# Kernel optimization log

Measured on AMD Instinct MI355X. Metric: run time of the kernel, lower is better.

Reference implementation:

```python
import jax, jax.numpy as jnp
import numpy as np

B, S, E, H = 2, 2048, 2048, 16
D = E // H

def setup_inputs() -> dict:
    key = jax.random.key(0)
    ks = jax.random.split(key, 9)
    sc = 1.0 / np.sqrt(E)
    return {
        "x":  jax.random.normal(ks[0], (B, S, E), jnp.float32),
        "Wq": jax.random.normal(ks[1], (E, E), jnp.float32) * sc,
        "bq": jax.random.normal(ks[2], (E,), jnp.float32) * 0.01,
        "Wk": jax.random.normal(ks[3], (E, E), jnp.float32) * sc,
        "bk": jax.random.normal(ks[4], (E,), jnp.float32) * 0.01,
        "Wv": jax.random.normal(ks[5], (E, E), jnp.float32) * sc,
        "bv": jax.random.normal(ks[6], (E,), jnp.float32) * 0.01,
        "Wo": jax.random.normal(ks[7], (E, E), jnp.float32) * sc,
        "bo": jax.random.normal(ks[8], (E,), jnp.float32) * 0.01,
    }

def _split_heads(t):
    # [B,S,E] -> [B,H,S,D]
    return t.reshape(B, S, H, D).transpose(0, 2, 1, 3)

def reference(x, Wq, bq, Wk, bk, Wv, bv, Wo, bo):
    # projections (nn.Linear: y = x @ W^T + b)
    q = _split_heads(x @ Wq.T + bq)
    k = _split_heads(x @ Wk.T + bk)
    v = _split_heads(x @ Wv.T + bv)

    # scaled causal attention; scale uses k.size(-1) == head_dim D
    scores = jnp.einsum("bhqd,bhkd->bhqk", q, k) / jnp.sqrt(jnp.asarray(D, q.dtype))
    causal = jnp.tril(jnp.ones((S, S), bool))  # [S,S]
    scores = jnp.where(causal[None, None, :, :], scores, -jnp.inf)
    # training path subtracts row max before softmax (no-op under stable softmax)
    scores = scores - jnp.max(scores, axis=-1, keepdims=True)
    attn = jax.nn.softmax(scores, axis=-1)
    # dropout_rate = 0.0 -> identity
    ctx = jnp.einsum("bhqk,bhkd->bhqd", attn, v)

    # merge heads [B,H,S,D] -> [B,S,E], final projection
    out = ctx.transpose(0, 2, 1, 3).reshape(B, S, E)
    return out @ Wo.T + bo
```

## Files before the change

kernel.cpp:

```cpp
#include <hip/hip_runtime.h>

typedef unsigned short u16;
typedef __attribute__((ext_vector_type(4))) float f32x4;
typedef __attribute__((ext_vector_type(8))) short s16x8;
typedef __attribute__((ext_vector_type(4))) unsigned short u16x4;

#define MFMA16(a, b, c) __builtin_amdgcn_mfma_f32_16x16x32_bf16((a), (b), (c), 0, 0, 0)

__device__ __forceinline__ u16 f2bf(float f) {
  union { float f; unsigned u; } v; v.f = f;
  unsigned u = v.u;
  u += 0x7fffu + ((u >> 16) & 1u);
  return (u16)(u >> 16);
}

__device__ __forceinline__ void gl_lds16(const void* g, void* l) {
  __builtin_amdgcn_global_load_lds(
      (const __attribute__((address_space(1))) void*)g,
      (__attribute__((address_space(3))) void*)l, 16, 0, 0);
}

__global__ void cast6(const float* __restrict__ x,
                      const float* __restrict__ w0, const float* __restrict__ w1,
                      const float* __restrict__ w2, const float* __restrict__ w3,
                      u16* __restrict__ ws) {
  const int y = blockIdx.y;
  const float* src;
  u16* dst;
  if (y < 2) { src = x + (size_t)y * 4194304; dst = ws + (size_t)y * 4194304; }
  else {
    src = (y == 2) ? w0 : (y == 3) ? w1 : (y == 4) ? w2 : w3;
    dst = ws + 8388608 + (size_t)(y - 2) * 4194304;
  }
  const int i = blockIdx.x * 256 + threadIdx.x;
  f32x4 v = ((const f32x4*)src)[i];
  u16x4 o;
#pragma unroll
  for (int e = 0; e < 4; ++e) o[e] = f2bf(v[e]);
  ((u16x4*)dst)[i] = o;
}

__global__ __launch_bounds__(256, 2) void gemm_qkv(
    const u16* __restrict__ A,
    const u16* __restrict__ W0, const u16* __restrict__ W1, const u16* __restrict__ W2,
    const float* __restrict__ b0, const float* __restrict__ b1, const float* __restrict__ b2,
    u16* __restrict__ Qo, u16* __restrict__ Ko, u16* __restrict__ Vo) {
  constexpr int Kd = 2048;
  __shared__ __align__(16) u16 smem[17408];
  u16* sA = smem;
  u16* sB = smem + 8192;
  const int z = blockIdx.z;
  const u16* Bw = (z == 0) ? W0 : (z == 1) ? W1 : W2;
  const float* bias = (z == 0) ? b0 : (z == 1) ? b1 : b2;

  const int tid = threadIdx.x;
  const int lane = tid & 63, w = tid >> 6;
  const int ln = lane & 15, quad = lane >> 4;
  const int m0 = blockIdx.y * 128, n0 = blockIdx.x * 128;
  const int wm = (w >> 1) * 64, wn = (w & 1) * 64;

  f32x4 acc[4][4] = {};
  const int srow = lane >> 3;
  const int scol = (lane & 7) * 8;

  for (int k0 = 0; k0 < Kd; k0 += 64) {
#pragma unroll
    for (int c = 0; c < 4; ++c) {
      const int chunk = c * 4 + w;
      const int row = chunk * 8 + srow;
      gl_lds16(A + (size_t)(m0 + row) * Kd + k0 + scol, (char*)sA + chunk * 1024);
      gl_lds16(Bw + (size_t)(n0 + row) * Kd + k0 + scol, (char*)sB + chunk * 1024);
    }
    __syncthreads();
#pragma unroll
    for (int kk = 0; kk < 64; kk += 32) {
      s16x8 af[4], bf[4];
#pragma unroll
      for (int t = 0; t < 4; ++t) {
        af[t] = *(const s16x8*)&sA[(wm + t * 16 + ln) * 64 + kk + quad * 8];
        bf[t] = *(const s16x8*)&sB[(wn + t * 16 + ln) * 64 + kk + quad * 8];
      }
#pragma unroll
      for (int tm = 0; tm < 4; ++tm)
#pragma unroll
        for (int tn = 0; tn < 4; ++tn)
          acc[tm][tn] = MFMA16(af[tm], bf[tn], acc[tm][tn]);
    }
    __syncthreads();
  }

  if (z < 2) {
    u16* out = (z == 0) ? Qo : Ko;
    const float scale = (z == 0) ? 0.08838834764831845f : 1.0f;
#pragma unroll
    for (int tn = 0; tn < 4; ++tn) {
      const int n = n0 + wn + tn * 16 + ln;
      const float bv = bias[n];
      const int h = n >> 7, d = n & 127;
#pragma unroll
      for (int tm = 0; tm < 4; ++tm)
#pragma unroll
        for (int r = 0; r < 4; ++r) {
          const int m = m0 + wm + tm * 16 + quad * 4 + r;
          const int b = m >> 11, s = m & 2047;
          out[(((size_t)(b * 16 + h)) << 18) + ((size_t)s << 7) + d] =
              f2bf((acc[tm][tn][r] + bv) * scale);
        }
    }
  } else {
    u16* Tt = smem;
#pragma unroll
    for (int tn = 0; tn < 4; ++tn) {
      const int n = n0 + wn + tn * 16 + ln;
      const float bv = bias[n];
      const int dl = wn + tn * 16 + ln;
#pragma unroll
      for (int tm = 0; tm < 4; ++tm)
#pragma unroll
        for (int r = 0; r < 4; ++r) {
          const int sl = wm + tm * 16 + quad * 4 + r;
          Tt[dl * 136 + sl] = f2bf(acc[tm][tn][r] + bv);
        }
    }
    __syncthreads();
    const int h = n0 >> 7, b = m0 >> 11, s0 = m0 & 2047;
#pragma unroll
    for (int c = 0; c < 8; ++c) {
      const int id = c * 256 + tid;
      const int row = id >> 4, cc = id & 15;
      s16x8 vr = *(const s16x8*)&Tt[row * 136 + cc * 8];
      *(s16x8*)&Vo[(((size_t)((b * 16 + h) * 128 + row)) << 11) + s0 + cc * 8] = vr;
    }
  }
}

__global__ __launch_bounds__(256, 2) void gemm_out(const u16* __restrict__ A,
                                                   const u16* __restrict__ Bw,
                                                   const float* __restrict__ bias,
                                                   float* __restrict__ out) {
  constexpr int Kd = 2048;
  __shared__ __align__(16) u16 sA[128 * 64];
  __shared__ __align__(16) u16 sB[128 * 64];
  const int tid = threadIdx.x;
  const int lane = tid & 63, w = tid >> 6;
  const int ln = lane & 15, quad = lane >> 4;
  const int m0 = blockIdx.y * 128, n0 = blockIdx.x * 128;
  const int wm = (w >> 1) * 64, wn = (w & 1) * 64;

  f32x4 acc[4][4] = {};
  const int srow = lane >> 3;
  const int scol = (lane & 7) * 8;

  for (int k0 = 0; k0 < Kd; k0 += 64) {
#pragma unroll
    for (int c = 0; c < 4; ++c) {
      const int chunk = c * 4 + w;
      const int row = chunk * 8 + srow;
      gl_lds16(A + (size_t)(m0 + row) * Kd + k0 + scol, (char*)sA + chunk * 1024);
      gl_lds16(Bw + (size_t)(n0 + row) * Kd + k0 + scol, (char*)sB + chunk * 1024);
    }
    __syncthreads();
#pragma unroll
    for (int kk = 0; kk < 64; kk += 32) {
      s16x8 af[4], bf[4];
#pragma unroll
      for (int t = 0; t < 4; ++t) {
        af[t] = *(const s16x8*)&sA[(wm + t * 16 + ln) * 64 + kk + quad * 8];
        bf[t] = *(const s16x8*)&sB[(wn + t * 16 + ln) * 64 + kk + quad * 8];
      }
#pragma unroll
      for (int tm = 0; tm < 4; ++tm)
#pragma unroll
        for (int tn = 0; tn < 4; ++tn)
          acc[tm][tn] = MFMA16(af[tm], bf[tn], acc[tm][tn]);
    }
    __syncthreads();
  }
#pragma unroll
  for (int tn = 0; tn < 4; ++tn) {
    const int n = n0 + wn + tn * 16 + ln;
    const float bv = bias[n];
#pragma unroll
    for (int tm = 0; tm < 4; ++tm)
#pragma unroll
      for (int r = 0; r < 4; ++r) {
        const int m = m0 + wm + tm * 16 + quad * 4 + r;
        out[(size_t)m * 2048 + n] = acc[tm][tn][r] + bv;
      }
  }
}

__global__ __launch_bounds__(256, 2) void attn_kernel(const u16* __restrict__ Q,
                                                      const u16* __restrict__ Kp,
                                                      const u16* __restrict__ Vt,
                                                      u16* __restrict__ ctx) {
  __shared__ __align__(16) u16 smem[24576];
  u16* sP = smem;
  u16* sK = smem + 8192;
  u16* sV = smem + 16384;

  const int flat = blockIdx.x + (blockIdx.y << 4);
  const int bh = flat >> 4;
  const int i = (flat < 256) ? (15 - (flat & 15)) : (flat & 15);
  const size_t base = (size_t)bh << 18;

  const int tid = threadIdx.x, lane = tid & 63, w = tid >> 6;
  const int ln = lane & 15, quad = lane >> 4, ln7 = lane & 7;

#pragma unroll
  for (int c = 0; c < 8; ++c) {
    const int chunk0 = (c * 4 + w) * 64;
    const int chunk = chunk0 + lane;
    const int row = chunk >> 4, cc = chunk & 15;
    gl_lds16(Q + base + (size_t)((i * 128 + row) * 128 + ((cc ^ (row & 15)) << 3)),
             (char*)sK + chunk0 * 16);
  }
  __syncthreads();
  s16x8 qf[2][4];
#pragma unroll
  for (int tm = 0; tm < 2; ++tm)
#pragma unroll
    for (int kc = 0; kc < 4; ++kc)
      qf[tm][kc] =
          *(const s16x8*)&sK[(w * 32 + tm * 16 + ln) * 128 + (((kc * 4 + quad) ^ ln) << 3)];
  __syncthreads();

  auto stageK = [&](int j) {
#pragma unroll
    for (int c = 0; c < 4; ++c) {
      const int chunk0 = (c * 4 + w) * 64;
      const int chunk = chunk0 + lane;
      const int row = chunk >> 4, cc = chunk & 15;
      gl_lds16(Kp + base + (size_t)((j * 64 + row) * 128 + ((cc ^ (row & 15)) << 3)),
               (char*)sK + chunk0 * 16);
    }
  };
  auto stageV = [&](int j) {
#pragma unroll
    for (int c = 0; c < 4; ++c) {
      const int chunk0 = (c * 4 + w) * 64;
      const int chunk = chunk0 + lane;
      const int row = chunk >> 3, cc = chunk & 7;
      gl_lds16(Vt + base + (size_t)(row * 2048 + j * 64 + ((cc ^ (row & 7)) << 3)),
               (char*)sV + chunk0 * 16);
    }
  };

  stageK(0);
  stageV(0);
  __syncthreads();

  f32x4 o_acc[2][8] = {};
  float lsum[2][4] = {};
  const int jmax = 2 * i + 1;

  for (int j = 0; j <= jmax; ++j) {
    f32x4 sacc[2][4] = {};
#pragma unroll
    for (int kc = 0; kc < 4; ++kc) {
      s16x8 kf[4];
#pragma unroll
      for (int tn = 0; tn < 4; ++tn)
        kf[tn] = *(const s16x8*)&sK[(tn * 16 + ln) * 128 + (((kc * 4 + quad) ^ ln) << 3)];
#pragma unroll
      for (int tm = 0; tm < 2; ++tm)
#pragma unroll
        for (int tn = 0; tn < 4; ++tn)
          sacc[tm][tn] = MFMA16(qf[tm][kc], kf[tn], sacc[tm][tn]);
    }

    const bool diag = (j >= 2 * i);
#pragma unroll
    for (int tm = 0; tm < 2; ++tm)
#pragma unroll
      for (int tn = 0; tn < 4; ++tn) {
        const int kg = j * 64 + tn * 16 + ln;
#pragma unroll
        for (int r = 0; r < 4; ++r) {
          const int rloc = w * 32 + tm * 16 + quad * 4 + r;
          float pv = __expf(sacc[tm][tn][r]);
          if (diag && kg > i * 128 + rloc) pv = 0.f;
          lsum[tm][r] += pv;
          const int chunk = tn * 2 + (ln >> 3);
          sP[rloc * 64 + ((chunk ^ (rloc & 7)) << 3) + ln7] = f2bf(pv);
        }
      }
    __syncthreads();
    if (j < jmax) stageK(j + 1);

#pragma unroll
    for (int kc = 0; kc < 2; ++kc) {
      s16x8 pf[2], vf[8];
#pragma unroll
      for (int tm = 0; tm < 2; ++tm)
        pf[tm] =
            *(const s16x8*)&sP[(w * 32 + tm * 16 + ln) * 64 + (((kc * 4 + quad) ^ ln7) << 3)];
#pragma unroll
      for (int tn = 0; tn < 8; ++tn)
        vf[tn] = *(const s16x8*)&sV[(tn * 16 + ln) * 64 + (((kc * 4 + quad) ^ ln7) << 3)];
#pragma unroll
      for (int tm = 0; tm < 2; ++tm)
#pragma unroll
        for (int tn = 0; tn < 8; ++tn)
          o_acc[tm][tn] = MFMA16(pf[tm], vf[tn], o_acc[tm][tn]);
    }
    __syncthreads();
    if (j < jmax) stageV(j + 1);
  }

  const int b = bh >> 4, h = bh & 15;
#pragma unroll
  for (int tm = 0; tm < 2; ++tm) {
    float rinv[4];
#pragma unroll
    for (int r = 0; r < 4; ++r) {
      float s = lsum[tm][r];
      s += __shfl_xor(s, 1);
      s += __shfl_xor(s, 2);
      s += __shfl_xor(s, 4);
      s += __shfl_xor(s, 8);
      rinv[r] = __builtin_amdgcn_rcpf(s);
    }
#pragma unroll
    for (int tn = 0; tn < 8; ++tn) {
      const int d = tn * 16 + ln;
#pragma unroll
      for (int r = 0; r < 4; ++r) {
        const int sg = i * 128 + w * 32 + tm * 16 + quad * 4 + r;
        ctx[((size_t)b << 22) + (size_t)sg * 2048 + h * 128 + d] =
            f2bf(o_acc[tm][tn][r] * rinv[r]);
      }
    }
  }
}

extern "C" void kernel_launch(void* const* d_in, const int* in_sizes, int n_in,
                              void* d_out, int out_size, void* d_ws, size_t ws_size,
                              hipStream_t stream) {
  const float* x = (const float*)d_in[0];
  const float* Wq = (const float*)d_in[1];
  const float* bq = (const float*)d_in[2];
  const float* Wk = (const float*)d_in[3];
  const float* bk = (const float*)d_in[4];
  const float* Wv = (const float*)d_in[5];
  const float* bv = (const float*)d_in[6];
  const float* Wo = (const float*)d_in[7];
  const float* bo = (const float*)d_in[8];

  u16* ws = (u16*)d_ws;
  u16* xb = ws;
  u16* Wqb = xb + 8388608;
  u16* Wkb = Wqb + 4194304;
  u16* Wvb = Wkb + 4194304;
  u16* Wob = Wvb + 4194304;
  u16* Qb = Wob + 4194304;
  u16* Kb = Qb + 8388608;
  u16* Vtb = Kb + 8388608;
  u16* ctxb = Vtb + 8388608;

  cast6<<<dim3(4096, 6), 256, 0, stream>>>(x, Wq, Wk, Wv, Wo, ws);

  gemm_qkv<<<dim3(16, 32, 3), 256, 0, stream>>>(xb, Wqb, Wkb, Wvb, bq, bk, bv, Qb, Kb, Vtb);

  attn_kernel<<<dim3(16, 32), 256, 0, stream>>>(Qb, Kb, Vtb, ctxb);

  gemm_out<<<dim3(16, 32), 256, 0, stream>>>(ctxb, Wob, bo, (float*)d_out);
}
```

Before: 391.8 us.

## Swap MFMA operand order for vectorized epilogues and XOR-swizzle GEMM LDS tiles

Measured after the change: 366.8 us. 6.4% less time.

```diff
diff --git a/kernel.cpp b/kernel.cpp
--- a/kernel.cpp
+++ b/kernel.cpp
@@ -40,13 +40,53 @@
   ((u16x4*)dst)[i] = o;
 }
 
+template <int SWAP>
+__device__ __forceinline__ void gemm_core(const u16* __restrict__ A,
+                                          const u16* __restrict__ Bw,
+                                          u16* sA, u16* sB,
+                                          f32x4 (&acc)[4][4],
+                                          int m0, int n0, int tid) {
+  const int lane = tid & 63, w = tid >> 6;
+  const int ln = lane & 15, quad = lane >> 4, ln7 = ln & 7;
+  const int wm = (w >> 1) * 64, wn = (w & 1) * 64;
+  const int srow = lane >> 3;
+  const int scol = (((lane & 7) ^ srow)) * 8;
+
+  for (int k0 = 0; k0 < 2048; k0 += 64) {
+#pragma unroll
+    for (int c = 0; c < 4; ++c) {
+      const int chunk = c * 4 + w;
+      const int row = chunk * 8 + srow;
+      gl_lds16(A + (size_t)(m0 + row) * 2048 + k0 + scol, (char*)sA + chunk * 1024);
+      gl_lds16(Bw + (size_t)(n0 + row) * 2048 + k0 + scol, (char*)sB + chunk * 1024);
+    }
+    __syncthreads();
+#pragma unroll
+    for (int kk = 0; kk < 64; kk += 32) {
+      s16x8 af[4], bf[4];
+      const int g = (kk >> 3) + quad;
+#pragma unroll
+      for (int t = 0; t < 4; ++t) {
+        af[t] = *(const s16x8*)&sA[(wm + t * 16 + ln) * 64 + ((g ^ ln7) << 3)];
+        bf[t] = *(const s16x8*)&sB[(wn + t * 16 + ln) * 64 + ((g ^ ln7) << 3)];
+      }
+#pragma unroll
+      for (int tm = 0; tm < 4; ++tm)
+#pragma unroll
+        for (int tn = 0; tn < 4; ++tn)
+          acc[tm][tn] = SWAP ? MFMA16(bf[tn], af[tm], acc[tm][tn])
+                             : MFMA16(af[tm], bf[tn], acc[tm][tn]);
+    }
+    __syncthreads();
+  }
+}
+
 __global__ __launch_bounds__(256, 2) void gemm_qkv(
     const u16* __restrict__ A,
     const u16* __restrict__ W0, const u16* __restrict__ W1, const u16* __restrict__ W2,
     const float* __restrict__ b0, const float* __restrict__ b1, const float* __restrict__ b2,
     u16* __restrict__ Qo, u16* __restrict__ Ko, u16* __restrict__ Vo) {
-  constexpr int Kd = 2048;
-  __shared__ __align__(16) u16 smem[17408];
+  __shared__ __align__(16) u16 smem[16384];
   u16* sA = smem;
   u16* sB = smem + 8192;
   const int z = blockIdx.z;
@@ -60,76 +100,41 @@
   const int wm = (w >> 1) * 64, wn = (w & 1) * 64;
 
   f32x4 acc[4][4] = {};
-  const int srow = lane >> 3;
-  const int scol = (lane & 7) * 8;
-
-  for (int k0 = 0; k0 < Kd; k0 += 64) {
-#pragma unroll
-    for (int c = 0; c < 4; ++c) {
-      const int chunk = c * 4 + w;
-      const int row = chunk * 8 + srow;
-      gl_lds16(A + (size_t)(m0 + row) * Kd + k0 + scol, (char*)sA + chunk * 1024);
-      gl_lds16(Bw + (size_t)(n0 + row) * Kd + k0 + scol, (char*)sB + chunk * 1024);
-    }
-    __syncthreads();
-#pragma unroll
-    for (int kk = 0; kk < 64; kk += 32) {
-      s16x8 af[4], bf[4];
-#pragma unroll
-      for (int t = 0; t < 4; ++t) {
-        af[t] = *(const s16x8*)&sA[(wm + t * 16 + ln) * 64 + kk + quad * 8];
-        bf[t] = *(const s16x8*)&sB[(wn + t * 16 + ln) * 64 + kk + quad * 8];
-      }
-#pragma unroll
-      for (int tm = 0; tm < 4; ++tm)
-#pragma unroll
-        for (int tn = 0; tn < 4; ++tn)
-          acc[tm][tn] = MFMA16(af[tm], bf[tn], acc[tm][tn]);
-    }
-    __syncthreads();
-  }
-
   if (z < 2) {
+    gemm_core<1>(A, Bw, sA, sB, acc, m0, n0, tid);
     u16* out = (z == 0) ? Qo : Ko;
     const float scale = (z == 0) ? 0.08838834764831845f : 1.0f;
+#pragma unroll
+    for (int tn = 0; tn < 4; ++tn) {
+      const int n_base = n0 + wn + tn * 16 + quad * 4;
+      const f32x4 bv = *(const f32x4*)&bias[n_base];
+      const int h = n_base >> 7, dl = n_base & 127;
+#pragma unroll
+      for (int tm = 0; tm < 4; ++tm) {
+        const int m = m0 + wm + tm * 16 + ln;
+        const int b = m >> 11, s = m & 2047;
+        u16x4 ov;
+#pragma unroll
+        for (int r = 0; r < 4; ++r) ov[r] = f2bf((acc[tm][tn][r] + bv[r]) * scale);
+        *(u16x4*)&out[(((size_t)(b * 16 + h)) << 18) + ((size_t)s << 7) + dl] = ov;
+      }
+    }
+  } else {
+    gemm_core<0>(A, Bw, sA, sB, acc, m0, n0, tid);
+    const int b = m0 >> 11;
 #pragma unroll
     for (int tn = 0; tn < 4; ++tn) {
       const int n = n0 + wn + tn * 16 + ln;
       const float bv = bias[n];
-      const int h = n >> 7, d = n & 127;
-#pragma unroll
-      for (int tm = 0; tm < 4; ++tm)
-#pragma unroll
-        for (int r = 0; r < 4; ++r) {
-          const int m = m0 + wm + tm * 16 + quad * 4 + r;
-          const int b = m >> 11, s = m & 2047;
-          out[(((size_t)(b * 16 + h)) << 18) + ((size_t)s << 7) + d] =
-              f2bf((acc[tm][tn][r] + bv) * scale);
-        }
-    }
-  } else {
-    u16* Tt = smem;
-#pragma unroll
-    for (int tn = 0; tn < 4; ++tn) {
-      const int n = n0 + wn + tn * 16 + ln;
-      const float bv = bias[n];
-      const int dl = wn + tn * 16 + ln;
-#pragma unroll
-      for (int tm = 0; tm < 4; ++tm)
-#pragma unroll
-        for (int r = 0; r < 4; ++r) {
-          const int sl = wm + tm * 16 + quad * 4 + r;
-          Tt[dl * 136 + sl] = f2bf(acc[tm][tn][r] + bv);
-        }
-    }
-    __syncthreads();
-    const int h = n0 >> 7, b = m0 >> 11, s0 = m0 & 2047;
-#pragma unroll
-    for (int c = 0; c < 8; ++c) {
-      const int id = c * 256 + tid;
-      const int row = id >> 4, cc = id & 15;
-      s16x8 vr = *(const s16x8*)&Tt[row * 136 + cc * 8];
-      *(s16x8*)&Vo[(((size_t)((b * 16 + h) * 128 + row)) << 11) + s0 + cc * 8] = vr;
+      const int h = n >> 7, dl = n & 127;
+#pragma unroll
+      for (int tm = 0; tm < 4; ++tm) {
+        const int s_base = (m0 & 2047) + wm + tm * 16 + quad * 4;
+        u16x4 ov;
+#pragma unroll
+        for (int r = 0; r < 4; ++r) ov[r] = f2bf(acc[tm][tn][r] + bv);
+        *(u16x4*)&Vo[(((size_t)((b * 16 + h) * 128 + dl)) << 11) + s_base] = ov;
+      }
     }
   }
 }
@@ -138,9 +143,9 @@
                                                    const u16* __restrict__ Bw,
                                                    const float* __restrict__ bias,
                                                    float* __restrict__ out) {
-  constexpr int Kd = 2048;
-  __shared__ __align__(16) u16 sA[128 * 64];
-  __shared__ __align__(16) u16 sB[128 * 64];
+  __shared__ __align__(16) u16 smem[16384];
+  u16* sA = smem;
+  u16* sB = smem + 8192;
   const int tid = threadIdx.x;
   const int lane = tid & 63, w = tid >> 6;
   const int ln = lane & 15, quad = lane >> 4;
@@ -148,45 +153,19 @@
   const int wm = (w >> 1) * 64, wn = (w & 1) * 64;
 
   f32x4 acc[4][4] = {};
-  const int srow = lane >> 3;
-  const int scol = (lane & 7) * 8;
-
-  for (int k0 = 0; k0 < Kd; k0 += 64) {
-#pragma unroll
-    for (int c = 0; c < 4; ++c) {
-      const int chunk = c * 4 + w;
-      const int row = chunk * 8 + srow;
-      gl_lds16(A + (size_t)(m0 + row) * Kd + k0 + scol, (char*)sA + chunk * 1024);
-      gl_lds16(Bw + (size_t)(n0 + row) * Kd + k0 + scol, (char*)sB + chunk * 1024);
-    }
-    __syncthreads();
-#pragma unroll
-    for (int kk = 0; kk < 64; kk += 32) {
-      s16x8 af[4], bf[4];
-#pragma unroll
-      for (int t = 0; t < 4; ++t) {
-        af[t] = *(const s16x8*)&sA[(wm + t * 16 + ln) * 64 + kk + quad * 8];
-        bf[t] = *(const s16x8*)&sB[(wn + t * 16 + ln) * 64 + kk + quad * 8];
-      }
-#pragma unroll
-      for (int tm = 0; tm < 4; ++tm)
-#pragma unroll
-        for (int tn = 0; tn < 4; ++tn)
-          acc[tm][tn] = MFMA16(af[tm], bf[tn], acc[tm][tn]);
-    }
-    __syncthreads();
-  }
+  gemm_core<1>(A, Bw, sA, sB, acc, m0, n0, tid);
 #pragma unroll
   for (int tn = 0; tn < 4; ++tn) {
-    const int n = n0 + wn + tn * 16 + ln;
-    const float bv = bias[n];
-#pragma unroll
-    for (int tm = 0; tm < 4; ++tm)
-#pragma unroll
-      for (int r = 0; r < 4; ++r) {
-        const int m = m0 + wm + tm * 16 + quad * 4 + r;
-        out[(size_t)m * 2048 + n] = acc[tm][tn][r] + bv;
-      }
+    const int n_base = n0 + wn + tn * 16 + quad * 4;
+    const f32x4 bv = *(const f32x4*)&bias[n_base];
+#pragma unroll
+    for (int tm = 0; tm < 4; ++tm) {
+      const int m = m0 + wm + tm * 16 + ln;
+      f32x4 ov;
+#pragma unroll
+      for (int r = 0; r < 4; ++r) ov[r] = acc[tm][tn][r] + bv[r];
+      *(f32x4*)&out[(size_t)m * 2048 + n_base] = ov;
+    }
   }
 }
 
@@ -218,11 +197,11 @@
   __syncthreads();
   s16x8 qf[2][4];
 #pragma unroll
-  for (int tm = 0; tm < 2; ++tm)
+  for (int qt = 0; qt < 2; ++qt)
 #pragma unroll
     for (int kc = 0; kc < 4; ++kc)
-      qf[tm][kc] =
-          *(const s16x8*)&sK[(w * 32 + tm * 16 + ln) * 128 + (((kc * 4 + quad) ^ ln) << 3)];
+      qf[qt][kc] =
+          *(const s16x8*)&sK[(w * 32 + qt * 16 + ln) * 128 + (((kc * 4 + quad) ^ ln) << 3)];
   __syncthreads();
 
   auto stageK = [&](int j) {
@@ -250,88 +229,89 @@
   stageV(0);
   __syncthreads();
 
-  f32x4 o_acc[2][8] = {};
-  float lsum[2][4] = {};
+  f32x4 o_acc[8][2] = {};
+  float lsum[2] = {0.f, 0.f};
   const int jmax = 2 * i + 1;
+  const int qg = i * 128 + w * 32 + ln;
 
   for (int j = 0; j <= jmax; ++j) {
-    f32x4 sacc[2][4] = {};
+    f32x4 sacc[4][2] = {};
 #pragma unroll
     for (int kc = 0; kc < 4; ++kc) {
       s16x8 kf[4];
 #pragma unroll
-      for (int tn = 0; tn < 4; ++tn)
-        kf[tn] = *(const s16x8*)&sK[(tn * 16 + ln) * 128 + (((kc * 4 + quad) ^ ln) << 3)];
-#pragma unroll
-      for (int tm = 0; tm < 2; ++tm)
-#pragma unroll
-        for (int tn = 0; tn < 4; ++tn)
-          sacc[tm][tn] = MFMA16(qf[tm][kc], kf[tn], sacc[tm][tn]);
+      for (int kt = 0; kt < 4; ++kt)
+        kf[kt] = *(const s16x8*)&sK[(kt * 16 + ln) * 128 + (((kc * 4 + quad) ^ ln) << 3)];
+#pragma unroll
+      for (int kt = 0; kt < 4; ++kt)
+#pragma unroll
+        for (int qt = 0; qt < 2; ++qt)
+          sacc[kt][qt] = MFMA16(kf[kt], qf[qt][kc], sacc[kt][qt]);
     }
 
     const bool diag = (j >= 2 * i);
 #pragma unroll
-    for (int tm = 0; tm < 2; ++tm)
-#pragma unroll
-      for (int tn = 0; tn < 4; ++tn) {
-        const int kg = j * 64 + tn * 16 + ln;
+    for (int kt = 0; kt < 4; ++kt)
+#pragma unroll
+      for (int qt = 0; qt < 2; ++qt) {
+        u16x4 pk;
 #pragma unroll
         for (int r = 0; r < 4; ++r) {
-          const int rloc = w * 32 + tm * 16 + quad * 4 + r;
-          float pv = __expf(sacc[tm][tn][r]);
-          if (diag && kg > i * 128 + rloc) pv = 0.f;
-          lsum[tm][r] += pv;
-          const int chunk = tn * 2 + (ln >> 3);
-          sP[rloc * 64 + ((chunk ^ (rloc & 7)) << 3) + ln7] = f2bf(pv);
+          const int kg = j * 64 + kt * 16 + quad * 4 + r;
+          float pv = __expf(sacc[kt][qt][r]);
+          if (diag && kg > qg + qt * 16) pv = 0.f;
+          lsum[qt] += pv;
+          pk[r] = f2bf(pv);
         }
+        const int qrow = w * 32 + qt * 16 + ln;
+        const int c = kt * 4 + quad;
+        *(u16x4*)&sP[qrow * 64 + ((c ^ (qrow & 14)) << 2)] = pk;
       }
     __syncthreads();
     if (j < jmax) stageK(j + 1);
 
 #pragma unroll
     for (int kc = 0; kc < 2; ++kc) {
-      s16x8 pf[2], vf[8];
-#pragma unroll
-      for (int tm = 0; tm < 2; ++tm)
-        pf[tm] =
-            *(const s16x8*)&sP[(w * 32 + tm * 16 + ln) * 64 + (((kc * 4 + quad) ^ ln7) << 3)];
-#pragma unroll
-      for (int tn = 0; tn < 8; ++tn)
-        vf[tn] = *(const s16x8*)&sV[(tn * 16 + ln) * 64 + (((kc * 4 + quad) ^ ln7) << 3)];
-#pragma unroll
-      for (int tm = 0; tm < 2; ++tm)
-#pragma unroll
-        for (int tn = 0; tn < 8; ++tn)
-          o_acc[tm][tn] = MFMA16(pf[tm], vf[tn], o_acc[tm][tn]);
+      s16x8 vf[8], pf[2];
+#pragma unroll
+      for (int qt = 0; qt < 2; ++qt) {
+        const int qrow = w * 32 + qt * 16 + ln;
+        const int c0 = kc * 8 + quad * 2;
+        pf[qt] = *(const s16x8*)&sP[qrow * 64 + ((c0 ^ (qrow & 14)) << 2)];
+      }
+#pragma unroll
+      for (int dt = 0; dt < 8; ++dt)
+        vf[dt] = *(const s16x8*)&sV[(dt * 16 + ln) * 64 + (((kc * 4 + quad) ^ ln7) << 3)];
+#pragma unroll
+      for (int dt = 0; dt < 8; ++dt)
+#pragma unroll
+        for (int qt = 0; qt < 2; ++qt)
+          o_acc[dt][qt] = MFMA16(vf[dt], pf[qt], o_acc[dt][qt]);
     }
     __syncthreads();
     if (j < jmax) stageV(j + 1);
   }
 
   const int b = bh >> 4, h = bh & 15;
-#pragma unroll
-  for (int tm = 0; tm < 2; ++tm) {
-    float rinv[4];
-#pragma unroll
-    for (int r = 0; r < 4; ++r) {
-      float s = lsum[tm][r];
-      s += __shfl_xor(s, 1);
-      s += __shfl_xor(s, 2);
-      s += __shfl_xor(s, 4);
-      s += __shfl_xor(s, 8);
-      rinv[r] = __builtin_amdgcn_rcpf(s);
-    }
-#pragma unroll
-    for (int tn = 0; tn < 8; ++tn) {
-      const int d = tn * 16 + ln;
-#pragma unroll
-      for (int r = 0; r < 4; ++r) {
-        const int sg = i * 128 + w * 32 + tm * 16 + quad * 4 + r;
-        ctx[((size_t)b << 22) + (size_t)sg * 2048 + h * 128 + d] =
-            f2bf(o_acc[tm][tn][r] * rinv[r]);
-      }
-    }
-  }
+  float rinv[2];
+#pragma unroll
+  for (int qt = 0; qt < 2; ++qt) {
+    float s = lsum[qt];
+    s += __shfl_xor(s, 16);
+    s += __shfl_xor(s, 32);
+    rinv[qt] = __builtin_amdgcn_rcpf(s);
+  }
+#pragma unroll
+  for (int dt = 0; dt < 8; ++dt)
+#pragma unroll
+    for (int qt = 0; qt < 2; ++qt) {
+      const int sg = i * 128 + w * 32 + qt * 16 + ln;
+      const int d0 = h * 128 + dt * 16 + quad * 4;
+      u16x4 ov;
+#pragma unroll
+      for (int r = 0; r < 4; ++r) ov[r] = f2bf(o_acc[dt][qt][r] * rinv[qt]);
+      *(u16x4*)&ctx[((size_t)b << 22) + (size_t)sg * 2048 + d0] = ov;
+    }
 }
 
 extern "C" void kernel_launch(void* const* d_in, const int* in_sizes, int n_in,
```
